# Optimization experiments

Measured on AMD Instinct MI355X. Metric: run time of the kernel, lower is better.

## Reference

```python
import jax, jax.numpy as jnp
import numpy as np

N_NODES = 100000
N_EDGES = 3200000
F_IN = 128
HID = 16


def gcn_conv(x, W, b, src, dst, n_nodes):
    # PyG GCNConv: h = x @ W; add self-loops; deg on dst; sym-normalized scatter-add; + bias
    h = x @ W  # [N, out]
    loop = jnp.arange(n_nodes, dtype=src.dtype)
    s = jnp.concatenate([src, loop])
    d = jnp.concatenate([dst, loop])
    ones = jnp.ones(s.shape[0], dtype=h.dtype)
    deg = jax.ops.segment_sum(ones, d, num_segments=n_nodes)  # in-degree incl self-loop
    dinv = jnp.where(deg > 0, jax.lax.rsqrt(deg), 0.0)
    norm = dinv[s] * dinv[d]  # [E+N]
    msg = h[s] * norm[:, None]
    out = jax.ops.segment_sum(msg, d, num_segments=n_nodes)
    return out + b


def setup_inputs() -> dict:
    key = jax.random.key(0)
    ks = jax.random.split(key, 8)
    x = jax.random.normal(ks[0], (N_NODES, F_IN), dtype=jnp.float32)
    edge_index = jax.random.randint(ks[1], (2, N_EDGES), 0, N_NODES, dtype=jnp.int32)
    sc1 = 1.0 / np.sqrt(F_IN)
    sc2 = 1.0 / np.sqrt(HID)
    sc3 = 1.0 / np.sqrt(2 * HID)
    W1 = jax.random.uniform(ks[2], (F_IN, HID), jnp.float32, -sc1, sc1)
    b1 = jnp.zeros((HID,), jnp.float32)
    W2 = jax.random.uniform(ks[3], (HID, HID), jnp.float32, -sc2, sc2)
    b2 = jnp.zeros((HID,), jnp.float32)
    Wf = jax.random.uniform(ks[4], (2 * HID, 1), jnp.float32, -sc3, sc3)
    bf = jax.random.uniform(ks[5], (1,), jnp.float32, -sc3, sc3)
    return {"x": x, "edge_index": edge_index, "W1": W1, "b1": b1, "W2": W2, "b2": b2, "Wf": Wf, "bf": bf}


def reference(x, edge_index, W1, b1, W2, b2, Wf, bf):
    src, dst = edge_index[0], edge_index[1]
    h = gcn_conv(x, W1, b1, src, dst, N_NODES)
    h = jax.nn.relu(h)  # dropout is identity in eval mode
    h = gcn_conv(h, W2, b2, src, dst, N_NODES)
    edge_emb = jnp.concatenate([h[src], h[dst]], axis=1)  # [E, 2*HID]
    pred = edge_emb @ Wf + bf  # [E, 1]
    return pred.squeeze(-1)
```

## Files before the change

### kernel.cpp

```cpp
#include <hip/hip_runtime.h>
#include <hip/hip_fp16.h>

#define N_NODES 100000
#define N_EDGES 3200000
#define F_IN 128
#define HID 16

#define SHIFT 8
#define NPB 256
#define NB 391
#define CHUNK 4096
#define NCHUNK ((N_EDGES + CHUNK - 1) / CHUNK)
#define MAXBE 9216
#define SMAX 18
#define CPAD 16

__device__ __forceinline__ float2 h2f(unsigned u) {
    __half2 h;
    *reinterpret_cast<unsigned*>(&h) = u;
    return __half22float2(h);
}
__device__ __forceinline__ unsigned f2h(float a, float b) {
    __half2 h = __floats2half2_rn(a, b);
    return *reinterpret_cast<unsigned*>(&h);
}

__global__ __launch_bounds__(512) void k_part(const int* __restrict__ src,
                                              const int* __restrict__ dst,
                                              int* __restrict__ cursor,
                                              unsigned* __restrict__ ebuf, int E) {
    __shared__ int lcnt[512];
    __shared__ int sc[512];
    __shared__ int lcur[512];
    __shared__ int dlt[512];
    __shared__ unsigned sbuf[CHUNK];
    __shared__ unsigned short sbkt[CHUNK];
    int t = threadIdx.x;
    lcnt[t] = 0;
    __syncthreads();
    int e0 = blockIdx.x * CHUNK;
    int ne = min(CHUNK, E - e0);
    for (int e = t; e < ne; e += 512) atomicAdd(&lcnt[dst[e0 + e] >> SHIFT], 1);
    __syncthreads();
    sc[t] = lcnt[t];
    __syncthreads();
#pragma unroll
    for (int o = 1; o < 512; o <<= 1) {
        int xv = (t >= o) ? sc[t - o] : 0;
        __syncthreads();
        sc[t] += xv;
        __syncthreads();
    }
    {
        int c = lcnt[t];
        int o = sc[t] - c;
        lcur[t] = o;
        if (t < NB && c) dlt[t] = t * MAXBE + atomicAdd(&cursor[t * CPAD], c) - o;
    }
    __syncthreads();
    for (int e = t; e < ne; e += 512) {
        int d = dst[e0 + e];
        int b = d >> SHIFT;
        int p = atomicAdd(&lcur[b], 1);
        sbuf[p] = ((unsigned)src[e0 + e] << SHIFT) | (unsigned)(d & (NPB - 1));
        sbkt[p] = (unsigned short)b;
    }
    __syncthreads();
    for (int k = t; k < ne; k += 512) ebuf[k + dlt[sbkt[k]]] = sbuf[k];
}

__global__ __launch_bounds__(512) void k_sort2(const unsigned* __restrict__ ebuf,
                                               const int* __restrict__ cursor,
                                               const float* __restrict__ x,
                                               const float* __restrict__ W1,
                                               int* __restrict__ ebuf2,
                                               int2* __restrict__ offse,
                                               float* __restrict__ dinv,
                                               uint4* __restrict__ gt, int N) {
    __shared__ int hist[NPB];
    __shared__ int sc2[NPB];
    __shared__ int cur[NPB];
    __shared__ int sbufS[MAXBE];
    __shared__ float w1s[F_IN * HID];
    int t = threadIdx.x;
    int b = blockIdx.x;
    for (int idx = t; idx < F_IN * HID; idx += 512) w1s[idx] = W1[idx];
    if (t < NPB) hist[t] = 0;
    __syncthreads();
    int cnt = min(cursor[b * CPAD], MAXBE);
    int base = b * MAXBE;
    unsigned eu[SMAX];
    int nq = 0;
    for (int e = t; e < cnt; e += 512) eu[nq++] = ebuf[base + e];
    for (int q = 0; q < nq; q++) atomicAdd(&hist[eu[q] & (NPB - 1u)], 1);
    __syncthreads();
    int v = (t < NPB) ? hist[t] : 0;
    if (t < NPB) sc2[t] = v;
    __syncthreads();
#pragma unroll
    for (int o = 1; o < NPB; o <<= 1) {
        int xv = (t < NPB && t >= o) ? sc2[t - o] : 0;
        __syncthreads();
        if (t < NPB) sc2[t] += xv;
        __syncthreads();
    }
    if (t < NPB) {
        int ex = sc2[t] - v;
        cur[t] = ex;
        int i = b * NPB + t;
        if (i < N) {
            offse[i] = make_int2(base + ex, base + ex + v);
            dinv[i] = rsqrtf((float)(v + 1));
        }
    }
    __syncthreads();
    for (int q = 0; q < nq; q++) {
        int p = atomicAdd(&cur[eu[q] & (NPB - 1u)], 1);
        sbufS[p] = (int)(eu[q] >> SHIFT);
    }
    __syncthreads();
    for (int k = t; k < cnt; k += 512) ebuf2[base + k] = sbufS[k];
    int r = t >> 1, hf = t & 1;
    int i = b * NPB + r;
    float acc[HID];
#pragma unroll
    for (int n = 0; n < HID; n++) acc[n] = 0.f;
    if (i < N) {
        const float4* xr = (const float4*)(x + (size_t)i * F_IN + hf * (F_IN / 2));
#pragma unroll 4
        for (int k4 = 0; k4 < F_IN / 8; k4++) {
            float4 xv = xr[k4];
            int k = hf * (F_IN / 2) + k4 * 4;
#pragma unroll
            for (int n = 0; n < HID; n++) {
                acc[n] += xv.x * w1s[(k + 0) * HID + n] + xv.y * w1s[(k + 1) * HID + n] +
                          xv.z * w1s[(k + 2) * HID + n] + xv.w * w1s[(k + 3) * HID + n];
            }
        }
    }
#pragma unroll
    for (int n = 0; n < HID; n++) acc[n] += __shfl_xor(acc[n], 1);
    if (hf == 0 && i < N) {
        float dv = rsqrtf((float)(hist[r] + 1));
        uint4 w0, w1;
        w0.x = f2h(acc[0] * dv, acc[1] * dv);
        w0.y = f2h(acc[2] * dv, acc[3] * dv);
        w0.z = f2h(acc[4] * dv, acc[5] * dv);
        w0.w = f2h(acc[6] * dv, acc[7] * dv);
        w1.x = f2h(acc[8] * dv, acc[9] * dv);
        w1.y = f2h(acc[10] * dv, acc[11] * dv);
        w1.z = f2h(acc[12] * dv, acc[13] * dv);
        w1.w = f2h(acc[14] * dv, acc[15] * dv);
        gt[2 * (size_t)i] = w0;
        gt[2 * (size_t)i + 1] = w1;
    }
}

__global__ __launch_bounds__(256) void k_gather1(const unsigned* __restrict__ gtu,
                                                 const int2* __restrict__ offse,
                                                 const int* __restrict__ ebuf2,
                                                 const float* __restrict__ dinv,
                                                 const float* __restrict__ b1,
                                                 unsigned* __restrict__ htu, int N) {
    int i = (blockIdx.x * 256 + threadIdx.x) >> 6;
    int lane = threadIdx.x & 63;
    if (i >= N) return;
    int eo = lane >> 3, s = lane & 7;
    int2 oe = offse[i];
    float2 a = make_float2(0.f, 0.f);
    for (int e = oe.x + eo; e < oe.y; e += 8) {
        int sv = ebuf2[e];
        float2 f = h2f(gtu[sv * 8 + s]);
        a.x += f.x;
        a.y += f.y;
    }
    a.x += __shfl_xor(a.x, 8);  a.y += __shfl_xor(a.y, 8);
    a.x += __shfl_xor(a.x, 16); a.y += __shfl_xor(a.y, 16);
    a.x += __shfl_xor(a.x, 32); a.y += __shfl_xor(a.y, 32);
    if (eo == 0) {
        float2 f = h2f(gtu[i * 8 + s]);
        a.x += f.x;
        a.y += f.y;
        float dv = dinv[i];
        float2 bb = ((const float2*)b1)[s];
        float o0 = fmaxf(dv * a.x + bb.x, 0.f);
        float o1 = fmaxf(dv * a.y + bb.y, 0.f);
        htu[i * 8 + s] = f2h(o0, o1);
    }
}

__global__ __launch_bounds__(256) void k_gemm2q(const uint4* __restrict__ ht,
                                                const float* __restrict__ W2,
                                                const float* __restrict__ dinv,
                                                const float* __restrict__ Wf,
                                                float2* __restrict__ q, int N) {
    __shared__ float w[HID * HID];
    __shared__ float wfs[32];
    w[threadIdx.x] = W2[threadIdx.x];
    if (threadIdx.x < 32) wfs[threadIdx.x] = Wf[threadIdx.x];
    __syncthreads();
    int i = blockIdx.x * 256 + threadIdx.x;
    if (i >= N) return;
    uint4 r0 = ht[2 * (size_t)i], r1 = ht[2 * (size_t)i + 1];
    float hv[HID];
    float2 f;
    f = h2f(r0.x); hv[0] = f.x; hv[1] = f.y;
    f = h2f(r0.y); hv[2] = f.x; hv[3] = f.y;
    f = h2f(r0.z); hv[4] = f.x; hv[5] = f.y;
    f = h2f(r0.w); hv[6] = f.x; hv[7] = f.y;
    f = h2f(r1.x); hv[8] = f.x; hv[9] = f.y;
    f = h2f(r1.y); hv[10] = f.x; hv[11] = f.y;
    f = h2f(r1.z); hv[12] = f.x; hv[13] = f.y;
    f = h2f(r1.w); hv[14] = f.x; hv[15] = f.y;
    float out[HID];
#pragma unroll
    for (int n = 0; n < HID; n++) out[n] = 0.f;
#pragma unroll
    for (int k = 0; k < HID; k++) {
#pragma unroll
        for (int n = 0; n < HID; n++) out[n] += hv[k] * w[k * HID + n];
    }
    float qs = 0.f, qd = 0.f;
#pragma unroll
    for (int n = 0; n < HID; n++) {
        qs += out[n] * wfs[n];
        qd += out[n] * wfs[16 + n];
    }
    float dv = dinv[i];
    q[i] = make_float2(qs * dv, qd * dv);
}

__global__ __launch_bounds__(256) void k_gather2(const float2* __restrict__ q,
                                                 const int2* __restrict__ offse,
                                                 const int* __restrict__ ebuf2,
                                                 const float* __restrict__ dinv,
                                                 const float* __restrict__ b2,
                                                 const float* __restrict__ Wf,
                                                 const float* __restrict__ bf,
                                                 float2* __restrict__ nd, int N) {
    __shared__ float2 C;
    if (threadIdx.x == 0) {
        float c1 = 0.f, c2 = 0.f;
#pragma unroll
        for (int k = 0; k < HID; k++) {
            c1 += b2[k] * Wf[k];
            c2 += b2[k] * Wf[16 + k];
        }
        C = make_float2(c1, c2 + bf[0]);
    }
    __syncthreads();
    int grp = threadIdx.x >> 4, l = threadIdx.x & 15;
    int i = blockIdx.x * 16 + grp;
    if (i >= N) return;
    int2 oe = offse[i];
    float2 a = make_float2(0.f, 0.f);
    for (int e = oe.x + l; e < oe.y; e += 16) {
        float2 qq = q[ebuf2[e]];
        a.x += qq.x;
        a.y += qq.y;
    }
    a.x += __shfl_xor(a.x, 1); a.y += __shfl_xor(a.y, 1);
    a.x += __shfl_xor(a.x, 2); a.y += __shfl_xor(a.y, 2);
    a.x += __shfl_xor(a.x, 4); a.y += __shfl_xor(a.y, 4);
    a.x += __shfl_xor(a.x, 8); a.y += __shfl_xor(a.y, 8);
    if (l == 0) {
        float2 self = q[i];
        float dv = dinv[i];
        nd[i] = make_float2(dv * (a.x + self.x) + C.x, dv * (a.y + self.y) + C.y);
    }
}

__global__ __launch_bounds__(256) void k_edge2(const int* __restrict__ src,
                                               const int* __restrict__ dst,
                                               const float2* __restrict__ nd,
                                               float* __restrict__ pred, int E) {
    int e = blockIdx.x * 256 + threadIdx.x;
    if (e >= E) return;
    pred[e] = nd[src[e]].x + nd[dst[e]].y;
}

extern "C" void kernel_launch(void* const* d_in, const int* in_sizes, int n_in,
                              void* d_out, int out_size, void* d_ws, size_t ws_size,
                              hipStream_t stream) {
    const float* x  = (const float*)d_in[0];
    const int*   ei = (const int*)d_in[1];
    const float* W1 = (const float*)d_in[2];
    const float* b1 = (const float*)d_in[3];
    const float* W2 = (const float*)d_in[4];
    const float* b2 = (const float*)d_in[5];
    const float* Wf = (const float*)d_in[6];
    const float* bf = (const float*)d_in[7];
    float* pred = (float*)d_out;

    const int N = N_NODES, E = N_EDGES;
    const int* src = ei;
    const int* dst = ei + E;

    char* w = (char*)d_ws;
    int*      cursor = (int*)(w + 0x0);
    float*    dinv   = (float*)(w + 0x10000);
    int2*     offse  = (int2*)(w + 0x80000);
    float2*   nd     = (float2*)(w + 0x150000);
    unsigned* ebuf   = (unsigned*)(w + 0x220000);
    float2*   q      = (float2*)(w + 0x220000);
    int*      ebuf2  = (int*)(w + 0x1000000);
    uint4*    gt     = (uint4*)(w + 0x1E00000);
    uint4*    ht     = (uint4*)(w + 0x2140000);

    const int B = 256;
    int gE   = (E + B - 1) / B;
    int gN   = (N + B - 1) / B;
    int gN64 = (N * 64) / B;
    int gN16 = (N + 15) / 16;

    hipMemsetAsync(cursor, 0, NB * CPAD * sizeof(int), stream);
    k_part<<<NCHUNK, 512, 0, stream>>>(src, dst, cursor, ebuf, E);
    k_sort2<<<NB, 512, 0, stream>>>(ebuf, cursor, x, W1, ebuf2, offse, dinv, gt, N);
    k_gather1<<<gN64, B, 0, stream>>>((const unsigned*)gt, offse, ebuf2, dinv, b1,
                                      (unsigned*)ht, N);
    k_gemm2q<<<gN, B, 0, stream>>>(ht, W2, dinv, Wf, q, N);
    k_gather2<<<gN16, B, 0, stream>>>(q, offse, ebuf2, dinv, b2, Wf, bf, nd, N);
    k_edge2<<<gE, B, 0, stream>>>(src, dst, nd, pred, E);
}
```

Before: 181.3 us.

## Split per-bucket sort into half-blocks, separate GEMM1 kernel, use wave-shuffle scans

The per-bucket counting sort now runs as two blocks per bucket, each sorting half the edges into its own region with separate offset arrays (offseA/offseB). The X·W1 projection moves into its own kernel that derives degree from both offset halves. Block-level prefix scans now use wave shuffles instead of log-step shared-memory scans. The goal is more parallelism and less shared memory per block in the sort, at the cost of an extra launch and two edge loops per node in the gathers. The workspace layout is reshuffled so gt aliases the ebuf region.

```diff
diff --git a/kernel.cpp b/kernel.cpp
--- a/kernel.cpp
+++ b/kernel.cpp
@@ -12,7 +12,8 @@
 #define CHUNK 4096
 #define NCHUNK ((N_EDGES + CHUNK - 1) / CHUNK)
 #define MAXBE 9216
-#define SMAX 18
+#define HALFR 4608
+#define SMAX 9
 #define CPAD 16
 
 __device__ __forceinline__ float2 h2f(unsigned u) {
@@ -30,33 +31,40 @@
                                               int* __restrict__ cursor,
                                               unsigned* __restrict__ ebuf, int E) {
     __shared__ int lcnt[512];
-    __shared__ int sc[512];
     __shared__ int lcur[512];
     __shared__ int dlt[512];
+    __shared__ int wsum[8], wpre[8];
     __shared__ unsigned sbuf[CHUNK];
     __shared__ unsigned short sbkt[CHUNK];
     int t = threadIdx.x;
+    int lane = t & 63, wid = t >> 6;
     lcnt[t] = 0;
     __syncthreads();
     int e0 = blockIdx.x * CHUNK;
     int ne = min(CHUNK, E - e0);
     for (int e = t; e < ne; e += 512) atomicAdd(&lcnt[dst[e0 + e] >> SHIFT], 1);
     __syncthreads();
-    sc[t] = lcnt[t];
-    __syncthreads();
-#pragma unroll
-    for (int o = 1; o < 512; o <<= 1) {
-        int xv = (t >= o) ? sc[t - o] : 0;
-        __syncthreads();
-        sc[t] += xv;
-        __syncthreads();
-    }
-    {
-        int c = lcnt[t];
-        int o = sc[t] - c;
-        lcur[t] = o;
-        if (t < NB && c) dlt[t] = t * MAXBE + atomicAdd(&cursor[t * CPAD], c) - o;
-    }
+    int v = lcnt[t];
+    int s = v;
+#pragma unroll
+    for (int o = 1; o < 64; o <<= 1) {
+        int u = __shfl_up(s, o);
+        if (lane >= o) s += u;
+    }
+    if (lane == 63) wsum[wid] = s;
+    __syncthreads();
+    if (t == 0) {
+        int r = 0;
+#pragma unroll
+        for (int k = 0; k < 8; k++) {
+            wpre[k] = r;
+            r += wsum[k];
+        }
+    }
+    __syncthreads();
+    int o = s + wpre[wid] - v;
+    lcur[t] = o;
+    if (t < NB && v) dlt[t] = t * MAXBE + atomicAdd(&cursor[t * CPAD], v) - o;
     __syncthreads();
     for (int e = t; e < ne; e += 512) {
         int d = dst[e0 + e];
@@ -69,48 +77,60 @@
     for (int k = t; k < ne; k += 512) ebuf[k + dlt[sbkt[k]]] = sbuf[k];
 }
 
-__global__ __launch_bounds__(512) void k_sort2(const unsigned* __restrict__ ebuf,
-                                               const int* __restrict__ cursor,
-                                               const float* __restrict__ x,
-                                               const float* __restrict__ W1,
-                                               int* __restrict__ ebuf2,
-                                               int2* __restrict__ offse,
-                                               float* __restrict__ dinv,
-                                               uint4* __restrict__ gt, int N) {
+__global__ __launch_bounds__(512) void k_sort2h(const unsigned* __restrict__ ebuf,
+                                                const int* __restrict__ cursor,
+                                                int* __restrict__ ebuf2,
+                                                int2* __restrict__ offseA,
+                                                int2* __restrict__ offseB, int N) {
     __shared__ int hist[NPB];
-    __shared__ int sc2[NPB];
     __shared__ int cur[NPB];
-    __shared__ int sbufS[MAXBE];
-    __shared__ float w1s[F_IN * HID];
+    __shared__ int wsum[4], wpre[4];
+    __shared__ int sbufS[HALFR];
     int t = threadIdx.x;
-    int b = blockIdx.x;
-    for (int idx = t; idx < F_IN * HID; idx += 512) w1s[idx] = W1[idx];
+    int lane = t & 63, wid = t >> 6;
+    int b = blockIdx.x >> 1, h = blockIdx.x & 1;
     if (t < NPB) hist[t] = 0;
     __syncthreads();
     int cnt = min(cursor[b * CPAD], MAXBE);
-    int base = b * MAXBE;
+    int mid = cnt >> 1;
+    int lo = h ? mid : 0;
+    int ne = (h ? cnt : mid) - lo;
+    int base_r = b * MAXBE + lo;
     unsigned eu[SMAX];
     int nq = 0;
-    for (int e = t; e < cnt; e += 512) eu[nq++] = ebuf[base + e];
+    for (int e = t; e < ne; e += 512) eu[nq++] = ebuf[base_r + e];
     for (int q = 0; q < nq; q++) atomicAdd(&hist[eu[q] & (NPB - 1u)], 1);
     __syncthreads();
+    int base_w = blockIdx.x * HALFR;
     int v = (t < NPB) ? hist[t] : 0;
-    if (t < NPB) sc2[t] = v;
-    __syncthreads();
-#pragma unroll
-    for (int o = 1; o < NPB; o <<= 1) {
-        int xv = (t < NPB && t >= o) ? sc2[t - o] : 0;
-        __syncthreads();
-        if (t < NPB) sc2[t] += xv;
-        __syncthreads();
-    }
     if (t < NPB) {
-        int ex = sc2[t] - v;
+        int s = v;
+#pragma unroll
+        for (int o = 1; o < 64; o <<= 1) {
+            int u = __shfl_up(s, o);
+            if (lane >= o) s += u;
+        }
+        if (lane == 63) wsum[wid] = s;
+        hist[t] = s;
+    }
+    __syncthreads();
+    if (t == 0) {
+        int r = 0;
+#pragma unroll
+        for (int k = 0; k < 4; k++) {
+            wpre[k] = r;
+            r += wsum[k];
+        }
+    }
+    __syncthreads();
+    if (t < NPB) {
+        int ex = hist[t] + wpre[wid] - v;
         cur[t] = ex;
         int i = b * NPB + t;
         if (i < N) {
-            offse[i] = make_int2(base + ex, base + ex + v);
-            dinv[i] = rsqrtf((float)(v + 1));
+            int2 oe = make_int2(base_w + ex, base_w + ex + v);
+            if (h == 0) offseA[i] = oe;
+            else        offseB[i] = oe;
         }
     }
     __syncthreads();
@@ -119,9 +139,21 @@
         sbufS[p] = (int)(eu[q] >> SHIFT);
     }
     __syncthreads();
-    for (int k = t; k < cnt; k += 512) ebuf2[base + k] = sbufS[k];
+    for (int k = t; k < ne; k += 512) ebuf2[base_w + k] = sbufS[k];
+}
+
+__global__ __launch_bounds__(256) void k_gemm1(const float* __restrict__ x,
+                                               const float* __restrict__ W1,
+                                               const int2* __restrict__ offseA,
+                                               const int2* __restrict__ offseB,
+                                               float* __restrict__ dinv,
+                                               uint4* __restrict__ gt, int N) {
+    __shared__ float w1s[F_IN * HID];
+    for (int idx = threadIdx.x; idx < F_IN * HID; idx += 256) w1s[idx] = W1[idx];
+    __syncthreads();
+    int t = threadIdx.x;
     int r = t >> 1, hf = t & 1;
-    int i = b * NPB + r;
+    int i = blockIdx.x * 128 + r;
     float acc[HID];
 #pragma unroll
     for (int n = 0; n < HID; n++) acc[n] = 0.f;
@@ -141,7 +173,10 @@
 #pragma unroll
     for (int n = 0; n < HID; n++) acc[n] += __shfl_xor(acc[n], 1);
     if (hf == 0 && i < N) {
-        float dv = rsqrtf((float)(hist[r] + 1));
+        int2 oA = offseA[i], oB = offseB[i];
+        int deg = (oA.y - oA.x) + (oB.y - oB.x);
+        float dv = rsqrtf((float)(deg + 1));
+        dinv[i] = dv;
         uint4 w0, w1;
         w0.x = f2h(acc[0] * dv, acc[1] * dv);
         w0.y = f2h(acc[2] * dv, acc[3] * dv);
@@ -157,7 +192,8 @@
 }
 
 __global__ __launch_bounds__(256) void k_gather1(const unsigned* __restrict__ gtu,
-                                                 const int2* __restrict__ offse,
+                                                 const int2* __restrict__ offseA,
+                                                 const int2* __restrict__ offseB,
                                                  const int* __restrict__ ebuf2,
                                                  const float* __restrict__ dinv,
                                                  const float* __restrict__ b1,
@@ -166,11 +202,15 @@
     int lane = threadIdx.x & 63;
     if (i >= N) return;
     int eo = lane >> 3, s = lane & 7;
-    int2 oe = offse[i];
+    int2 oA = offseA[i], oB = offseB[i];
     float2 a = make_float2(0.f, 0.f);
-    for (int e = oe.x + eo; e < oe.y; e += 8) {
-        int sv = ebuf2[e];
-        float2 f = h2f(gtu[sv * 8 + s]);
+    for (int e = oA.x + eo; e < oA.y; e += 8) {
+        float2 f = h2f(gtu[ebuf2[e] * 8 + s]);
+        a.x += f.x;
+        a.y += f.y;
+    }
+    for (int e = oB.x + eo; e < oB.y; e += 8) {
+        float2 f = h2f(gtu[ebuf2[e] * 8 + s]);
         a.x += f.x;
         a.y += f.y;
     }
@@ -231,7 +271,8 @@
 }
 
 __global__ __launch_bounds__(256) void k_gather2(const float2* __restrict__ q,
-                                                 const int2* __restrict__ offse,
+                                                 const int2* __restrict__ offseA,
+                                                 const int2* __restrict__ offseB,
                                                  const int* __restrict__ ebuf2,
                                                  const float* __restrict__ dinv,
                                                  const float* __restrict__ b2,
@@ -252,9 +293,14 @@
     int grp = threadIdx.x >> 4, l = threadIdx.x & 15;
     int i = blockIdx.x * 16 + grp;
     if (i >= N) return;
-    int2 oe = offse[i];
+    int2 oA = offseA[i], oB = offseB[i];
     float2 a = make_float2(0.f, 0.f);
-    for (int e = oe.x + l; e < oe.y; e += 16) {
+    for (int e = oA.x + l; e < oA.y; e += 16) {
+        float2 qq = q[ebuf2[e]];
+        a.x += qq.x;
+        a.y += qq.y;
+    }
+    for (int e = oB.x + l; e < oB.y; e += 16) {
         float2 qq = q[ebuf2[e]];
         a.x += qq.x;
         a.y += qq.y;
@@ -299,26 +345,29 @@
     char* w = (char*)d_ws;
     int*      cursor = (int*)(w + 0x0);
     float*    dinv   = (float*)(w + 0x10000);
-    int2*     offse  = (int2*)(w + 0x80000);
-    float2*   nd     = (float2*)(w + 0x150000);
-    unsigned* ebuf   = (unsigned*)(w + 0x220000);
-    float2*   q      = (float2*)(w + 0x220000);
-    int*      ebuf2  = (int*)(w + 0x1000000);
-    uint4*    gt     = (uint4*)(w + 0x1E00000);
-    uint4*    ht     = (uint4*)(w + 0x2140000);
+    int2*     offseA = (int2*)(w + 0x80000);
+    int2*     offseB = (int2*)(w + 0x150000);
+    float2*   nd     = (float2*)(w + 0x220000);
+    unsigned* ebuf   = (unsigned*)(w + 0x3C0000);
+    uint4*    gt     = (uint4*)(w + 0x3C0000);
+    float2*   q      = (float2*)(w + 0x700000);
+    int*      ebuf2  = (int*)(w + 0x11A0000);
+    uint4*    ht     = (uint4*)(w + 0x1F70000);
 
     const int B = 256;
     int gE   = (E + B - 1) / B;
     int gN   = (N + B - 1) / B;
+    int gN2  = (N + 127) / 128;
     int gN64 = (N * 64) / B;
     int gN16 = (N + 15) / 16;
 
     hipMemsetAsync(cursor, 0, NB * CPAD * sizeof(int), stream);
     k_part<<<NCHUNK, 512, 0, stream>>>(src, dst, cursor, ebuf, E);
-    k_sort2<<<NB, 512, 0, stream>>>(ebuf, cursor, x, W1, ebuf2, offse, dinv, gt, N);
-    k_gather1<<<gN64, B, 0, stream>>>((const unsigned*)gt, offse, ebuf2, dinv, b1,
+    k_sort2h<<<2 * NB, 512, 0, stream>>>(ebuf, cursor, ebuf2, offseA, offseB, N);
+    k_gemm1<<<gN2, B, 0, stream>>>(x, W1, offseA, offseB, dinv, gt, N);
+    k_gather1<<<gN64, B, 0, stream>>>((const unsigned*)gt, offseA, offseB, ebuf2, dinv, b1,
                                       (unsigned*)ht, N);
     k_gemm2q<<<gN, B, 0, stream>>>(ht, W2, dinv, Wf, q, N);
-    k_gather2<<<gN16, B, 0, stream>>>(q, offse, ebuf2, dinv, b2, Wf, bf, nd, N);
+    k_gather2<<<gN16, B, 0, stream>>>(q, offseA, offseB, ebuf2, dinv, b2, Wf, bf, nd, N);
     k_edge2<<<gE, B, 0, stream>>>(src, dst, nd, pred, E);
 }
```

After: 186.0 us. 1.03x slower.
